# Kernel optimization log

Measured on AMD Instinct MI355X. Metric: run time of the kernel, lower is better.

Reference implementation:

```python
import math
import jax, jax.numpy as jnp
import numpy as np


def setup_inputs() -> dict:
    key = jax.random.key(0)
    k1, k2 = jax.random.split(key)
    B, Sq, Sk, H, Hkv, D = 2, 2048, 2048, 16, 8, 128
    q = jax.random.normal(k1, (B, Sq, H, D), dtype=jnp.float32)
    kv = jax.random.normal(k2, (B, Sk, 2, Hkv, D), dtype=jnp.float32)
    return {"q": q, "kv": kv}


def reference(q, kv):
    # q: [B, Sq, H, D]; kv: [B, Sk, 2, Hkv, D]
    B, Sq, H, D = q.shape
    Sk = kv.shape[1]
    Hkv = kv.shape[3]
    if Hkv != H:
        # GQA: repeat each kv head g times consecutively ('... hkv d -> ... (hkv g) d')
        kv = jnp.repeat(kv, H // Hkv, axis=3)
    k = kv[:, :, 0]  # [B, Sk, H, D]
    v = kv[:, :, 1]  # [B, Sk, H, D]
    q = q.astype(jnp.float32)
    k = k.astype(jnp.float32)
    scale = 1.0 / math.sqrt(D)
    # scores: [B, H, Sq, Sk]
    scores = jnp.einsum('bqhd,bkhd->bhqk', q, k * scale)
    # causal mask with right-alignment offset: mask where col > row + Sk - Sq
    rows = jnp.arange(Sq)[:, None]
    cols = jnp.arange(Sk)[None, :]
    causal_mask = cols > rows + (Sk - Sq)  # [Sq, Sk]
    scores = jnp.where(causal_mask[None, None], jnp.float32(-10000.0), scores)
    attention = jax.nn.softmax(scores, axis=-1).astype(v.dtype)
    # output: [B, Sq, H, D]
    out = jnp.einsum('bhqk,bkhd->bqhd', attention, v)
    return out
```

## Files before the change

kernel.cpp:

```cpp
#include <hip/hip_runtime.h>
#include <stdint.h>


#define SQ 2048
#define SK 2048
#define NH 16
#define NKV 8
#define DH 128
#define KVSTRIDE (2*NKV*DH)
#define SCALE_LOG2E 0.12751743f

typedef __attribute__((ext_vector_type(8))) short bf8;
typedef __attribute__((ext_vector_type(4))) float f4;

__device__ __forceinline__ float fast_exp2(float x) {
  return __builtin_amdgcn_exp2f(x);
}

__device__ __forceinline__ short f2bf(float f) {
  uint32_t u = __builtin_bit_cast(uint32_t, f);
  u += 0x7FFFu + ((u >> 16) & 1u);
  return (short)(u >> 16);
}

__device__ __forceinline__ bf8 pack8(f4 a, f4 b) {
  bf8 v;
  v[0] = f2bf(a[0]); v[1] = f2bf(a[1]); v[2] = f2bf(a[2]); v[3] = f2bf(a[3]);
  v[4] = f2bf(b[0]); v[5] = f2bf(b[1]); v[6] = f2bf(b[2]); v[7] = f2bf(b[3]);
  return v;
}
__device__ __forceinline__ bf8 pack8s(f4 a, f4 b, float s) {
  bf8 v;
  v[0] = f2bf(a[0]*s); v[1] = f2bf(a[1]*s); v[2] = f2bf(a[2]*s); v[3] = f2bf(a[3]*s);
  v[4] = f2bf(b[0]*s); v[5] = f2bf(b[1]*s); v[6] = f2bf(b[2]*s); v[7] = f2bf(b[3]*s);
  return v;
}

template<int CTRL>
__device__ __forceinline__ float dppmov(float x) {
  int xi = __builtin_bit_cast(int, x);
  int r = __builtin_amdgcn_update_dpp(xi, xi, CTRL, 0xF, 0xF, false);
  return __builtin_bit_cast(float, r);
}
__device__ __forceinline__ float rowsum16(float v) {
  v += dppmov<0x121>(v);
  v += dppmov<0x122>(v);
  v += dppmov<0x124>(v);
  v += dppmov<0x128>(v);
  return v;
}
__device__ __forceinline__ float rowmax16(float v) {
  v = fmaxf(v, dppmov<0x121>(v));
  v = fmaxf(v, dppmov<0x122>(v));
  v = fmaxf(v, dppmov<0x124>(v));
  v = fmaxf(v, dppmov<0x128>(v));
  return v;
}

__device__ __forceinline__ void g2l16(const short* g, short* l) {
  __builtin_amdgcn_global_load_lds(
      (const __attribute__((address_space(1))) uint32_t*)g,
      (__attribute__((address_space(3))) uint32_t*)l, 16, 0, 0);
}

__global__ void conv_kv(const float* __restrict__ kv,
                        short* __restrict__ Kb, short* __restrict__ Vb) {
  int id = blockIdx.x * 256 + threadIdx.x;
  if (blockIdx.y == 0) {
    int c   = id & 15;
    int key = (id >> 4) & 63;
    int kt  = (id >> 10) & 31;
    int hk  = (id >> 15) & 7;
    int b   = (id >> 18) & 1;
    const float* src = kv + ((size_t)(b * SK + kt * 64 + key) * 2) * (NKV * DH)
                          + hk * DH + c * 8;
    f4 a = *(const f4*)src;
    f4 bb = *(const f4*)(src + 4);
    short* dst = Kb + ((size_t)((b * 8 + hk) * 32 + kt)) * 8192;
    *(bf8*)&dst[(key * 16 + (c ^ (key & 7))) * 8] = pack8(a, bb);
  } else {
    int d  = id & 127;
    int c  = (id >> 7) & 7;
    int kt = (id >> 10) & 31;
    int hk = (id >> 15) & 7;
    int b  = (id >> 18) & 1;
    const float* src = kv + ((size_t)(b * SK + kt * 64 + c * 8) * 2 + 1) * (NKV * DH)
                          + hk * DH + d;
    bf8 v;
#pragma unroll
    for (int kk = 0; kk < 8; ++kk) v[kk] = f2bf(src[(size_t)kk * KVSTRIDE]);
    short* dst = Vb + ((size_t)((b * 8 + hk) * 32 + kt)) * 8192;
    *(bf8*)&dst[(d * 8 + (c ^ (d & 7))) * 8] = v;
  }
}

__launch_bounds__(512, 2)
__global__ void fa_fwd3(const float* __restrict__ q,
                        const short* __restrict__ Kb,
                        const short* __restrict__ Vb,
                        float* __restrict__ out) {
  __shared__ __align__(16) short lsK[2][8192];
  __shared__ __align__(16) short lsV[2][8192];
  __shared__ __align__(16) short lsP[8][1536];

  const int tid  = threadIdx.x;
  const int w    = tid >> 6;
  const int l    = tid & 63;
  const int l15  = l & 15;
  const int quad = l >> 4;

  const int bx  = blockIdx.x;
  const int p   = bx >> 4;
  const int bhk = bx & 15;
  const int b   = bhk >> 3;
  const int hk  = bhk & 7;
  const int head  = hk * 2 + (w >> 2);
  const int rbase = (w & 3) * 16;

  const short* ktiles = Kb + ((size_t)((b * 8 + hk) * 32)) * 8192;
  const short* vtiles = Vb + ((size_t)((b * 8 + hk) * 32)) * 8192;
  short* myP = lsP[w];

  auto stage = [&](int kt, int nb) {
    const short* ks = ktiles + (size_t)kt * 8192 + tid * 8;
    const short* vs = vtiles + (size_t)kt * 8192 + tid * 8;
#pragma unroll
    for (int i = 0; i < 2; ++i) {
      g2l16(ks + i * 4096, &lsK[nb][i * 4096 + tid * 8]);
      g2l16(vs + i * 4096, &lsV[nb][i * 4096 + tid * 8]);
    }
  };

#pragma unroll 1
  for (int phase = 0; phase < 2; ++phase) {
    const int qt = phase ? (31 - p) : p;
    const int q0 = qt * 64;

    bf8 qf[4];
    {
      int row = q0 + rbase + l15;
      const float* qr = q + ((size_t)(b * SQ + row) * NH + head) * DH;
#pragma unroll
      for (int kc = 0; kc < 4; ++kc) {
        const float* src = qr + kc * 32 + quad * 8;
        f4 a = *(const f4*)src;
        f4 c = *(const f4*)(src + 4);
        qf[kc] = pack8s(a, c, SCALE_LOG2E);
      }
    }

    f4 O[8];
#pragma unroll
    for (int nt = 0; nt < 8; ++nt) O[nt] = (f4){0.f, 0.f, 0.f, 0.f};
    float lpart[4] = {0.f, 0.f, 0.f, 0.f};

    if (phase) __syncthreads();
    stage(0, 0);

    for (int kt = 0; kt <= qt; ++kt) {
      const int cur = kt & 1;
      __syncthreads();
      if (kt < qt) stage(kt + 1, cur ^ 1);

      f4 S[4];
#pragma unroll
      for (int nt = 0; nt < 4; ++nt) S[nt] = (f4){0.f, 0.f, 0.f, 0.f};
#pragma unroll
      for (int kc = 0; kc < 4; ++kc) {
#pragma unroll
        for (int nt = 0; nt < 4; ++nt) {
          int key = nt * 16 + l15;
          int c   = kc * 4 + quad;
          bf8 kf = *(const bf8*)&lsK[cur][(key * 16 + (c ^ (key & 7))) * 8];
          S[nt] = __builtin_amdgcn_mfma_f32_16x16x32_bf16(qf[kc], kf, S[nt], 0, 0, 0);
        }
      }

      if (kt == qt) {
#pragma unroll
        for (int nt = 0; nt < 4; ++nt)
#pragma unroll
          for (int r = 0; r < 4; ++r) {
            int rloc = rbase + quad * 4 + r;
            int kloc = nt * 16 + l15;
            if (kloc > rloc) S[nt][r] = -1e30f;
          }
      }

#pragma unroll
      for (int nt = 0; nt < 4; ++nt)
#pragma unroll
        for (int r = 0; r < 4; ++r) {
          float pe = fast_exp2(S[nt][r]);
          S[nt][r] = pe;
          lpart[r] += pe;
        }

#pragma unroll
      for (int r = 0; r < 4; ++r) {
        int m = quad * 4 + r;
#pragma unroll
        for (int nt = 0; nt < 4; ++nt) {
          int key = nt * 16 + l15;
          myP[(m * 8 + ((key >> 3) ^ (m & 7))) * 8 + (key & 7)] = f2bf(S[nt][r]);
        }
      }

#pragma unroll
      for (int kc = 0; kc < 2; ++kc) {
        int c = kc * 4 + quad;
        bf8 pf = *(const bf8*)&myP[(l15 * 8 + (c ^ (l15 & 7))) * 8];
#pragma unroll
        for (int nt = 0; nt < 8; ++nt) {
          int d = nt * 16 + l15;
          bf8 vf = *(const bf8*)&lsV[cur][(d * 8 + (c ^ (d & 7))) * 8];
          O[nt] = __builtin_amdgcn_mfma_f32_16x16x32_bf16(pf, vf, O[nt], 0, 0, 0);
        }
      }
    }

#pragma unroll
    for (int r = 0; r < 4; ++r) {
      float linv = 1.0f / rowsum16(lpart[r]);
      int row = q0 + rbase + quad * 4 + r;
      float* dst = out + ((size_t)(b * SQ + row) * NH + head) * DH + l15;
#pragma unroll
      for (int nt = 0; nt < 8; ++nt) dst[nt * 16] = O[nt][r] * linv;
    }
  }
}

__launch_bounds__(256, 2)
__global__ void fa_fwd_v1(const float* __restrict__ q,
                          const float* __restrict__ kv,
                          float* __restrict__ out) {
  __shared__ __align__(16) short lsK[64 * 128];
  __shared__ __align__(16) short lsV[128 * 64];
  __shared__ __align__(16) short lsP[4][32 * 64];

  const int tid  = threadIdx.x;
  const int w    = tid >> 6;
  const int l    = tid & 63;
  const int l15  = l & 15;
  const int quad = l >> 4;

  const int bx  = blockIdx.x;
  const int qt  = 31 - (bx >> 4);
  const int bhk = bx & 15;
  const int b   = bhk >> 3;
  const int hk  = bhk & 7;
  const int head  = hk * 2 + (w >> 1);
  const int mrow0 = (w & 1) * 32;
  const int q0    = qt * 64;

  const float* kbase = kv + (size_t)b * SK * KVSTRIDE + (size_t)hk * DH;
  const float* vbase = kbase + NKV * DH;

  bf8 qf[2][4];
#pragma unroll
  for (int mt = 0; mt < 2; ++mt)
#pragma unroll
    for (int kc = 0; kc < 4; ++kc) {
      int row = q0 + mrow0 + mt * 16 + l15;
      int d0  = kc * 32 + quad * 8;
      const float* src = q + ((size_t)(b * SQ + row) * NH + head) * DH + d0;
      f4 a = *(const f4*)src;
      f4 c = *(const f4*)(src + 4);
      qf[mt][kc] = pack8s(a, c, SCALE_LOG2E);
    }

  f4 O[2][8];
  float mrow[2][4], lrow[2][4];
#pragma unroll
  for (int mt = 0; mt < 2; ++mt) {
#pragma unroll
    for (int nt = 0; nt < 8; ++nt) O[mt][nt] = (f4){0.f, 0.f, 0.f, 0.f};
#pragma unroll
    for (int r = 0; r < 4; ++r) { mrow[mt][r] = -1e30f; lrow[mt][r] = 0.f; }
  }

  for (int kt = 0; kt <= qt; ++kt) {
    if (kt) __syncthreads();
    const int k0 = kt * 64;
#pragma unroll
    for (int i = 0; i < 4; ++i) {
      int id  = i * 256 + tid;
      int key = id >> 4;
      int c   = id & 15;
      const float* src = kbase + (size_t)(k0 + key) * KVSTRIDE + c * 8;
      f4 a = *(const f4*)src;
      f4 bb = *(const f4*)(src + 4);
      *(bf8*)&lsK[(key * 16 + (c ^ (key & 7))) * 8] = pack8(a, bb);
    }
#pragma unroll
    for (int i = 0; i < 4; ++i) {
      int u  = i * 4 + w;
      int kg = u >> 1;
      int d  = (u & 1) * 64 + l;
      const float* src = vbase + (size_t)(k0 + kg * 8) * KVSTRIDE + d;
      bf8 v;
#pragma unroll
      for (int kk = 0; kk < 8; ++kk) v[kk] = f2bf(src[(size_t)kk * KVSTRIDE]);
      *(bf8*)&lsV[(d * 8 + (kg ^ (d & 7))) * 8] = v;
    }
    __syncthreads();

    f4 S[2][4];
#pragma unroll
    for (int mt = 0; mt < 2; ++mt)
#pragma unroll
      for (int nt = 0; nt < 4; ++nt) S[mt][nt] = (f4){0.f, 0.f, 0.f, 0.f};
#pragma unroll
    for (int kc = 0; kc < 4; ++kc)
#pragma unroll
      for (int nt = 0; nt < 4; ++nt) {
        int key = nt * 16 + l15;
        int c   = kc * 4 + quad;
        bf8 kf = *(const bf8*)&lsK[(key * 16 + (c ^ (key & 7))) * 8];
        S[0][nt] = __builtin_amdgcn_mfma_f32_16x16x32_bf16(qf[0][kc], kf, S[0][nt], 0, 0, 0);
        S[1][nt] = __builtin_amdgcn_mfma_f32_16x16x32_bf16(qf[1][kc], kf, S[1][nt], 0, 0, 0);
      }

    if (kt == qt) {
#pragma unroll
      for (int mt = 0; mt < 2; ++mt)
#pragma unroll
        for (int nt = 0; nt < 4; ++nt)
#pragma unroll
          for (int r = 0; r < 4; ++r) {
            int rloc = mrow0 + mt * 16 + quad * 4 + r;
            int kloc = nt * 16 + l15;
            if (kloc > rloc) S[mt][nt][r] = -1e30f;
          }
    }

#pragma unroll
    for (int mt = 0; mt < 2; ++mt)
#pragma unroll
      for (int r = 0; r < 4; ++r) {
        float mx = fmaxf(fmaxf(S[mt][0][r], S[mt][1][r]),
                         fmaxf(S[mt][2][r], S[mt][3][r]));
        mx = rowmax16(mx);
        float mold = mrow[mt][r];
        float mnew = fmaxf(mold, mx);
        float alpha = fast_exp2(mold - mnew);
        mrow[mt][r] = mnew;
        float rs = 0.f;
#pragma unroll
        for (int nt = 0; nt < 4; ++nt) {
          float pe = fast_exp2(S[mt][nt][r] - mnew);
          S[mt][nt][r] = pe;
          rs += pe;
        }
        rs = rowsum16(rs);
        lrow[mt][r] = lrow[mt][r] * alpha + rs;
#pragma unroll
        for (int nt = 0; nt < 8; ++nt) O[mt][nt][r] *= alpha;
        int m = mt * 16 + quad * 4 + r;
#pragma unroll
        for (int nt = 0; nt < 4; ++nt) {
          int key = nt * 16 + l15;
          lsP[w][(m * 8 + ((key >> 3) ^ (m & 7))) * 8 + (key & 7)] =
              f2bf(S[mt][nt][r]);
        }
      }

#pragma unroll
    for (int kc = 0; kc < 2; ++kc) {
      bf8 pf[2];
#pragma unroll
      for (int mt = 0; mt < 2; ++mt) {
        int m = mt * 16 + l15;
        int c = kc * 4 + quad;
        pf[mt] = *(const bf8*)&lsP[w][(m * 8 + (c ^ (m & 7))) * 8];
      }
#pragma unroll
      for (int nt = 0; nt < 8; ++nt) {
        int d = nt * 16 + l15;
        int c = kc * 4 + quad;
        bf8 vf = *(const bf8*)&lsV[(d * 8 + (c ^ (d & 7))) * 8];
        O[0][nt] = __builtin_amdgcn_mfma_f32_16x16x32_bf16(pf[0], vf, O[0][nt], 0, 0, 0);
        O[1][nt] = __builtin_amdgcn_mfma_f32_16x16x32_bf16(pf[1], vf, O[1][nt], 0, 0, 0);
      }
    }
  }

#pragma unroll
  for (int mt = 0; mt < 2; ++mt)
#pragma unroll
    for (int r = 0; r < 4; ++r) {
      float linv = 1.0f / lrow[mt][r];
      int row = q0 + mrow0 + mt * 16 + quad * 4 + r;
      float* dst = out + ((size_t)(b * SQ + row) * NH + head) * DH + l15;
#pragma unroll
      for (int nt = 0; nt < 8; ++nt) dst[nt * 16] = O[mt][nt][r] * linv;
    }
}

extern "C" void kernel_launch(void* const* d_in, const int* in_sizes, int n_in,
                              void* d_out, int out_size, void* d_ws, size_t ws_size,
                              hipStream_t stream) {
  const float* q  = (const float*)d_in[0];
  const float* kv = (const float*)d_in[1];
  float* out      = (float*)d_out;
  (void)in_sizes; (void)n_in; (void)out_size;

  const size_t kb_elems = (size_t)2 * 8 * 32 * 8192;
  const size_t need = 2 * kb_elems * sizeof(short);

  if (ws_size >= need) {
    short* Kb = (short*)d_ws;
    short* Vb = Kb + kb_elems;
    conv_kv<<<dim3(2048, 2), 256, 0, stream>>>(kv, Kb, Vb);
    fa_fwd3<<<dim3(256), dim3(512), 0, stream>>>(q, Kb, Vb, out);
  } else {
    fa_fwd_v1<<<dim3(512), dim3(256), 0, stream>>>(q, kv, out);
  }
}
```

Before: 155.6 us.

## Give each wave two 16-row query tiles and launch one block per q-tile

Replaces the 512-thread, two-phase paired-q-tile kernel with a 256-thread kernel where each wave computes 32 query rows (two MFMA m-tiles) that share each K and V fragment loaded from LDS. The grid doubles to 512 blocks, each handling a single q tile, ordered from heaviest to lightest to balance the causal work. It also adds s_setprio around the MFMA sections and interleaves the exp/P-store with the PV matmul per k-chunk. This is meant to halve LDS reads per MFMA and improve scheduling, at the cost of more registers per wave, fewer waves per block, and dropping the explicit pairing of q tiles.

```diff
diff --git a/kernel.cpp b/kernel.cpp
--- a/kernel.cpp
+++ b/kernel.cpp
@@ -94,14 +94,14 @@
   }
 }
 
-__launch_bounds__(512, 2)
-__global__ void fa_fwd3(const float* __restrict__ q,
+__launch_bounds__(256, 2)
+__global__ void fa_fwd4(const float* __restrict__ q,
                         const short* __restrict__ Kb,
                         const short* __restrict__ Vb,
                         float* __restrict__ out) {
   __shared__ __align__(16) short lsK[2][8192];
   __shared__ __align__(16) short lsV[2][8192];
-  __shared__ __align__(16) short lsP[8][1536];
+  __shared__ __align__(16) short lsP[4][1024];
 
   const int tid  = threadIdx.x;
   const int w    = tid >> 6;
@@ -110,12 +110,14 @@
   const int quad = l >> 4;
 
   const int bx  = blockIdx.x;
-  const int p   = bx >> 4;
+  const int s   = bx >> 4;
+  const int qt  = (s < 16) ? (31 - s) : (s - 16);
   const int bhk = bx & 15;
   const int b   = bhk >> 3;
   const int hk  = bhk & 7;
-  const int head  = hk * 2 + (w >> 2);
-  const int rbase = (w & 3) * 16;
+  const int head  = hk * 2 + (w & 1);
+  const int mrow0 = (w >> 1) * 32;
+  const int q0    = qt * 64;
 
   const short* ktiles = Kb + ((size_t)((b * 8 + hk) * 32)) * 8192;
   const short* vtiles = Vb + ((size_t)((b * 8 + hk) * 32)) * 8192;
@@ -125,109 +127,119 @@
     const short* ks = ktiles + (size_t)kt * 8192 + tid * 8;
     const short* vs = vtiles + (size_t)kt * 8192 + tid * 8;
 #pragma unroll
-    for (int i = 0; i < 2; ++i) {
-      g2l16(ks + i * 4096, &lsK[nb][i * 4096 + tid * 8]);
-      g2l16(vs + i * 4096, &lsV[nb][i * 4096 + tid * 8]);
+    for (int i = 0; i < 4; ++i) {
+      g2l16(ks + i * 2048, &lsK[nb][i * 2048 + tid * 8]);
+      g2l16(vs + i * 2048, &lsV[nb][i * 2048 + tid * 8]);
     }
   };
 
+  bf8 qf[2][4];
+#pragma unroll
+  for (int mt = 0; mt < 2; ++mt) {
+    int row = q0 + mrow0 + mt * 16 + l15;
+    const float* qr = q + ((size_t)(b * SQ + row) * NH + head) * DH;
+#pragma unroll
+    for (int kc = 0; kc < 4; ++kc) {
+      const float* src = qr + kc * 32 + quad * 8;
+      f4 a = *(const f4*)src;
+      f4 c = *(const f4*)(src + 4);
+      qf[mt][kc] = pack8s(a, c, SCALE_LOG2E);
+    }
+  }
+
+  f4 O[2][8];
+#pragma unroll
+  for (int mt = 0; mt < 2; ++mt)
+#pragma unroll
+    for (int nt = 0; nt < 8; ++nt) O[mt][nt] = (f4){0.f, 0.f, 0.f, 0.f};
+  float lpart[2][4] = {{0.f, 0.f, 0.f, 0.f}, {0.f, 0.f, 0.f, 0.f}};
+
+  stage(0, 0);
+
 #pragma unroll 1
-  for (int phase = 0; phase < 2; ++phase) {
-    const int qt = phase ? (31 - p) : p;
-    const int q0 = qt * 64;
-
-    bf8 qf[4];
-    {
-      int row = q0 + rbase + l15;
-      const float* qr = q + ((size_t)(b * SQ + row) * NH + head) * DH;
-#pragma unroll
-      for (int kc = 0; kc < 4; ++kc) {
-        const float* src = qr + kc * 32 + quad * 8;
-        f4 a = *(const f4*)src;
-        f4 c = *(const f4*)(src + 4);
-        qf[kc] = pack8s(a, c, SCALE_LOG2E);
-      }
-    }
-
-    f4 O[8];
-#pragma unroll
-    for (int nt = 0; nt < 8; ++nt) O[nt] = (f4){0.f, 0.f, 0.f, 0.f};
-    float lpart[4] = {0.f, 0.f, 0.f, 0.f};
-
-    if (phase) __syncthreads();
-    stage(0, 0);
-
-    for (int kt = 0; kt <= qt; ++kt) {
-      const int cur = kt & 1;
-      __syncthreads();
-      if (kt < qt) stage(kt + 1, cur ^ 1);
-
-      f4 S[4];
-#pragma unroll
-      for (int nt = 0; nt < 4; ++nt) S[nt] = (f4){0.f, 0.f, 0.f, 0.f};
-#pragma unroll
-      for (int kc = 0; kc < 4; ++kc) {
-#pragma unroll
-        for (int nt = 0; nt < 4; ++nt) {
-          int key = nt * 16 + l15;
-          int c   = kc * 4 + quad;
-          bf8 kf = *(const bf8*)&lsK[cur][(key * 16 + (c ^ (key & 7))) * 8];
-          S[nt] = __builtin_amdgcn_mfma_f32_16x16x32_bf16(qf[kc], kf, S[nt], 0, 0, 0);
+  for (int kt = 0; kt <= qt; ++kt) {
+    const int cur = kt & 1;
+    __syncthreads();
+    if (kt < qt) stage(kt + 1, cur ^ 1);
+
+    f4 S[2][4];
+#pragma unroll
+    for (int mt = 0; mt < 2; ++mt)
+#pragma unroll
+      for (int nt = 0; nt < 4; ++nt) S[mt][nt] = (f4){0.f, 0.f, 0.f, 0.f};
+    __builtin_amdgcn_s_setprio(1);
+#pragma unroll
+    for (int kc = 0; kc < 4; ++kc) {
+#pragma unroll
+      for (int nt = 0; nt < 4; ++nt) {
+        int key = nt * 16 + l15;
+        int c   = kc * 4 + quad;
+        bf8 kf = *(const bf8*)&lsK[cur][(key * 16 + (c ^ (key & 7))) * 8];
+        S[0][nt] = __builtin_amdgcn_mfma_f32_16x16x32_bf16(qf[0][kc], kf, S[0][nt], 0, 0, 0);
+        S[1][nt] = __builtin_amdgcn_mfma_f32_16x16x32_bf16(qf[1][kc], kf, S[1][nt], 0, 0, 0);
+      }
+    }
+    __builtin_amdgcn_s_setprio(0);
+
+    if (kt == qt) {
+#pragma unroll
+      for (int mt = 0; mt < 2; ++mt)
+#pragma unroll
+        for (int nt = 0; nt < 4; ++nt)
+#pragma unroll
+          for (int r = 0; r < 4; ++r) {
+            int rloc = mrow0 + mt * 16 + quad * 4 + r;
+            int kloc = nt * 16 + l15;
+            if (kloc > rloc) S[mt][nt][r] = -1e30f;
+          }
+    }
+
+#pragma unroll
+    for (int kc = 0; kc < 2; ++kc) {
+#pragma unroll
+      for (int mt = 0; mt < 2; ++mt)
+#pragma unroll
+        for (int ntl = 0; ntl < 2; ++ntl) {
+          int nt = kc * 2 + ntl;
+#pragma unroll
+          for (int r = 0; r < 4; ++r) {
+            float pe = fast_exp2(S[mt][nt][r]);
+            lpart[mt][r] += pe;
+            int m  = mt * 16 + quad * 4 + r;
+            int kk = ntl * 16 + l15;
+            myP[(m * 4 + ((kk >> 3) ^ ((m >> 2) & 3))) * 8 + (kk & 7)] = f2bf(pe);
+          }
         }
-      }
-
-      if (kt == qt) {
-#pragma unroll
-        for (int nt = 0; nt < 4; ++nt)
-#pragma unroll
-          for (int r = 0; r < 4; ++r) {
-            int rloc = rbase + quad * 4 + r;
-            int kloc = nt * 16 + l15;
-            if (kloc > rloc) S[nt][r] = -1e30f;
-          }
-      }
-
-#pragma unroll
-      for (int nt = 0; nt < 4; ++nt)
-#pragma unroll
-        for (int r = 0; r < 4; ++r) {
-          float pe = fast_exp2(S[nt][r]);
-          S[nt][r] = pe;
-          lpart[r] += pe;
-        }
-
-#pragma unroll
-      for (int r = 0; r < 4; ++r) {
-        int m = quad * 4 + r;
-#pragma unroll
-        for (int nt = 0; nt < 4; ++nt) {
-          int key = nt * 16 + l15;
-          myP[(m * 8 + ((key >> 3) ^ (m & 7))) * 8 + (key & 7)] = f2bf(S[nt][r]);
-        }
-      }
-
-#pragma unroll
-      for (int kc = 0; kc < 2; ++kc) {
+
+      bf8 pf[2];
+#pragma unroll
+      for (int mt = 0; mt < 2; ++mt) {
+        int m = mt * 16 + l15;
+        pf[mt] = *(const bf8*)&myP[(m * 4 + (quad ^ ((m >> 2) & 3))) * 8];
+      }
+      __builtin_amdgcn_s_setprio(1);
+#pragma unroll
+      for (int nt = 0; nt < 8; ++nt) {
+        int d = nt * 16 + l15;
         int c = kc * 4 + quad;
-        bf8 pf = *(const bf8*)&myP[(l15 * 8 + (c ^ (l15 & 7))) * 8];
-#pragma unroll
-        for (int nt = 0; nt < 8; ++nt) {
-          int d = nt * 16 + l15;
-          bf8 vf = *(const bf8*)&lsV[cur][(d * 8 + (c ^ (d & 7))) * 8];
-          O[nt] = __builtin_amdgcn_mfma_f32_16x16x32_bf16(pf, vf, O[nt], 0, 0, 0);
-        }
-      }
-    }
-
+        bf8 vf = *(const bf8*)&lsV[cur][(d * 8 + (c ^ (d & 7))) * 8];
+        O[0][nt] = __builtin_amdgcn_mfma_f32_16x16x32_bf16(pf[0], vf, O[0][nt], 0, 0, 0);
+        O[1][nt] = __builtin_amdgcn_mfma_f32_16x16x32_bf16(pf[1], vf, O[1][nt], 0, 0, 0);
+      }
+      __builtin_amdgcn_s_setprio(0);
+    }
+  }
+
+#pragma unroll
+  for (int mt = 0; mt < 2; ++mt)
 #pragma unroll
     for (int r = 0; r < 4; ++r) {
-      float linv = 1.0f / rowsum16(lpart[r]);
-      int row = q0 + rbase + quad * 4 + r;
+      float linv = 1.0f / rowsum16(lpart[mt][r]);
+      int row = q0 + mrow0 + mt * 16 + quad * 4 + r;
       float* dst = out + ((size_t)(b * SQ + row) * NH + head) * DH + l15;
 #pragma unroll
-      for (int nt = 0; nt < 8; ++nt) dst[nt * 16] = O[nt][r] * linv;
-    }
-  }
+      for (int nt = 0; nt < 8; ++nt) dst[nt * 16] = O[mt][nt][r] * linv;
+    }
 }
 
 __launch_bounds__(256, 2)
@@ -412,7 +424,7 @@
     short* Kb = (short*)d_ws;
     short* Vb = Kb + kb_elems;
     conv_kv<<<dim3(2048, 2), 256, 0, stream>>>(kv, Kb, Vb);
-    fa_fwd3<<<dim3(256), dim3(512), 0, stream>>>(q, Kb, Vb, out);
+    fa_fwd4<<<dim3(512), dim3(256), 0, stream>>>(q, Kb, Vb, out);
   } else {
     fa_fwd_v1<<<dim3(512), dim3(256), 0, stream>>>(q, kv, out);
   }
```

Measured after the change: 161.5 us. 1.04x slower.

## Compute S transposed and feed P to PV MFMA from registers, skipping LDS round-trip

Applied to the files above, without the earlier changes.

Swaps the MFMA operands so QK^T yields S^T, and permutes the key order in the K conversion so each lane's accumulator values line up with the B-operand layout of the PV MFMA. P is then packed straight to bf16 with v_cvt_pk_bf16_f32 and used from registers, which removes the per-tile LDS store and reload of P. The causal mask and row-sum reduction are rewritten for the transposed layout. A padding shared array stays in place, presumably to keep occupancy unchanged.

```diff
diff --git a/kernel.cpp b/kernel.cpp
--- a/kernel.cpp
+++ b/kernel.cpp
@@ -12,6 +12,7 @@
 
 typedef __attribute__((ext_vector_type(8))) short bf8;
 typedef __attribute__((ext_vector_type(4))) float f4;
+typedef __attribute__((ext_vector_type(4))) int i4;
 
 __device__ __forceinline__ float fast_exp2(float x) {
   return __builtin_amdgcn_exp2f(x);
@@ -21,6 +22,12 @@
   uint32_t u = __builtin_bit_cast(uint32_t, f);
   u += 0x7FFFu + ((u >> 16) & 1u);
   return (short)(u >> 16);
+}
+
+__device__ __forceinline__ int cvtpk(float lo, float hi) {
+  int r;
+  asm("v_cvt_pk_bf16_f32 %0, %1, %2" : "=v"(r) : "v"(lo), "v"(hi));
+  return r;
 }
 
 __device__ __forceinline__ bf8 pack8(f4 a, f4 b) {
@@ -77,7 +84,8 @@
     f4 a = *(const f4*)src;
     f4 bb = *(const f4*)(src + 4);
     short* dst = Kb + ((size_t)((b * 8 + hk) * 32 + kt)) * 8192;
-    *(bf8*)&dst[(key * 16 + (c ^ (key & 7))) * 8] = pack8(a, bb);
+    int akey = (key & 0x23) | ((key & 4) << 2) | ((key & 0x18) >> 1);
+    *(bf8*)&dst[(akey * 16 + (c ^ (akey & 7))) * 8] = pack8(a, bb);
   } else {
     int d  = id & 127;
     int c  = (id >> 7) & 7;
@@ -95,13 +103,14 @@
 }
 
 __launch_bounds__(512, 2)
-__global__ void fa_fwd3(const float* __restrict__ q,
+__global__ void fa_fwd5(const float* __restrict__ q,
                         const short* __restrict__ Kb,
                         const short* __restrict__ Vb,
                         float* __restrict__ out) {
   __shared__ __align__(16) short lsK[2][8192];
   __shared__ __align__(16) short lsV[2][8192];
-  __shared__ __align__(16) short lsP[8][1536];
+  __shared__ __align__(16) short lsPad[12288];
+  if (q == nullptr) lsPad[threadIdx.x] = 0;
 
   const int tid  = threadIdx.x;
   const int w    = tid >> 6;
@@ -119,7 +128,6 @@
 
   const short* ktiles = Kb + ((size_t)((b * 8 + hk) * 32)) * 8192;
   const short* vtiles = Vb + ((size_t)((b * 8 + hk) * 32)) * 8192;
-  short* myP = lsP[w];
 
   auto stage = [&](int kt, int nb) {
     const short* ks = ktiles + (size_t)kt * 8192 + tid * 8;
@@ -152,7 +160,7 @@
     f4 O[8];
 #pragma unroll
     for (int nt = 0; nt < 8; ++nt) O[nt] = (f4){0.f, 0.f, 0.f, 0.f};
-    float lpart[4] = {0.f, 0.f, 0.f, 0.f};
+    float lpart = 0.f;
 
     if (phase) __syncthreads();
     stage(0, 0);
@@ -169,10 +177,10 @@
       for (int kc = 0; kc < 4; ++kc) {
 #pragma unroll
         for (int nt = 0; nt < 4; ++nt) {
-          int key = nt * 16 + l15;
+          int row = nt * 16 + l15;
           int c   = kc * 4 + quad;
-          bf8 kf = *(const bf8*)&lsK[cur][(key * 16 + (c ^ (key & 7))) * 8];
-          S[nt] = __builtin_amdgcn_mfma_f32_16x16x32_bf16(qf[kc], kf, S[nt], 0, 0, 0);
+          bf8 kf = *(const bf8*)&lsK[cur][(row * 16 + (c ^ (row & 7))) * 8];
+          S[nt] = __builtin_amdgcn_mfma_f32_16x16x32_bf16(kf, qf[kc], S[nt], 0, 0, 0);
         }
       }
 
@@ -181,9 +189,8 @@
         for (int nt = 0; nt < 4; ++nt)
 #pragma unroll
           for (int r = 0; r < 4; ++r) {
-            int rloc = rbase + quad * 4 + r;
-            int kloc = nt * 16 + l15;
-            if (kloc > rloc) S[nt][r] = -1e30f;
+            int kphys = ((nt >> 1) << 5) + (quad << 3) + ((nt & 1) << 2) + r;
+            if (kphys > rbase + l15) S[nt][r] = -1e30f;
           }
       }
 
@@ -193,35 +200,40 @@
         for (int r = 0; r < 4; ++r) {
           float pe = fast_exp2(S[nt][r]);
           S[nt][r] = pe;
-          lpart[r] += pe;
+          lpart += pe;
         }
 
-#pragma unroll
-      for (int r = 0; r < 4; ++r) {
-        int m = quad * 4 + r;
-#pragma unroll
-        for (int nt = 0; nt < 4; ++nt) {
-          int key = nt * 16 + l15;
-          myP[(m * 8 + ((key >> 3) ^ (m & 7))) * 8 + (key & 7)] = f2bf(S[nt][r]);
-        }
-      }
-
+      bf8 pf[2];
 #pragma unroll
       for (int kc = 0; kc < 2; ++kc) {
-        int c = kc * 4 + quad;
-        bf8 pf = *(const bf8*)&myP[(l15 * 8 + (c ^ (l15 & 7))) * 8];
+        i4 wv;
+        wv[0] = cvtpk(S[2*kc][0],   S[2*kc][1]);
+        wv[1] = cvtpk(S[2*kc][2],   S[2*kc][3]);
+        wv[2] = cvtpk(S[2*kc+1][0], S[2*kc+1][1]);
+        wv[3] = cvtpk(S[2*kc+1][2], S[2*kc+1][3]);
+        pf[kc] = __builtin_bit_cast(bf8, wv);
+      }
+
+#pragma unroll
+      for (int kc = 0; kc < 2; ++kc) {
 #pragma unroll
         for (int nt = 0; nt < 8; ++nt) {
           int d = nt * 16 + l15;
+          int c = kc * 4 + quad;
           bf8 vf = *(const bf8*)&lsV[cur][(d * 8 + (c ^ (d & 7))) * 8];
-          O[nt] = __builtin_amdgcn_mfma_f32_16x16x32_bf16(pf, vf, O[nt], 0, 0, 0);
+          O[nt] = __builtin_amdgcn_mfma_f32_16x16x32_bf16(pf[kc], vf, O[nt], 0, 0, 0);
         }
       }
     }
 
+    float lsum = lpart;
+    lsum += __shfl_xor(lsum, 16);
+    lsum += __shfl_xor(lsum, 32);
+
 #pragma unroll
     for (int r = 0; r < 4; ++r) {
-      float linv = 1.0f / rowsum16(lpart[r]);
+      float lr   = __shfl(lsum, quad * 4 + r);
+      float linv = 1.0f / lr;
       int row = q0 + rbase + quad * 4 + r;
       float* dst = out + ((size_t)(b * SQ + row) * NH + head) * DH + l15;
 #pragma unroll
@@ -412,7 +424,7 @@
     short* Kb = (short*)d_ws;
     short* Vb = Kb + kb_elems;
     conv_kv<<<dim3(2048, 2), 256, 0, stream>>>(kv, Kb, Vb);
-    fa_fwd3<<<dim3(256), dim3(512), 0, stream>>>(q, Kb, Vb, out);
+    fa_fwd5<<<dim3(256), dim3(512), 0, stream>>>(q, Kb, Vb, out);
   } else {
     fa_fwd_v1<<<dim3(512), dim3(256), 0, stream>>>(q, kv, out);
   }
```

Measured after the change: 146.6 us. 5.8% less time.
